# Kernel tuning notes

Hardware: AMD Instinct MI355X
Metric: run time of the kernel (lower is better)

The kernel has to match this reference:

```python
import jax, jax.numpy as jnp
import numpy as np

PI = 3.141592653589793
TAU = 2.0      # tau for both rpe_lif (spikingjelly default 2.0) and act_conv (params['tau'])
V_TH = 1.0     # spikingjelly LIFNode default v_threshold
EPS = 1e-5     # LayerNorm / BatchNorm eps


@jax.custom_vjp
def atan_spike(x):
    # Heaviside forward, ATan surrogate backward (spikingjelly surrogate.ATan, alpha=2)
    return (x >= 0.0).astype(x.dtype)

def _atan_fwd(x):
    return atan_spike(x), x

def _atan_bwd(x, g):
    # (alpha/2) / (1 + ((pi/2)*alpha*x)^2) with alpha=2 -> 1/(1+(pi*x)^2)
    return (g / (1.0 + (PI * x) ** 2),)

atan_spike.defvjp(_atan_fwd, _atan_bwd)


def lif(x_seq, tau=TAU):
    """Multi-step LIF: decay_input=True, v_reset=0, hard reset, detach_reset.
    x_seq: [T, ...]; returns spikes [T, ...]."""
    def step(v, x):
        v = v + (x - v) / tau                      # neuronal charge
        s = atan_spike(v - V_TH)                   # fire
        v = v * (1.0 - jax.lax.stop_gradient(s))   # detached hard reset to 0
        return v, s
    _, spikes = jax.lax.scan(step, jnp.zeros_like(x_seq[0]), x_seq)
    return spikes


def setup_inputs() -> dict:
    key = jax.random.key(0)
    ks = jax.random.split(key, 8)
    B, L, D, T = 256, 50, 128, 4
    n_items, n_h, n_v = 100001, 8, 4
    emb = jax.random.normal(ks[0], (n_items, D), jnp.float32) * 0.5
    emb = emb.at[0].set(0.0)  # padding_idx=0
    return {
        "item_seq": jax.random.randint(ks[1], (B, L), 0, n_items, jnp.int32),
        "emb_table": emb,
        "ln_gamma": jnp.ones((D,), jnp.float32),
        "ln_beta": jnp.zeros((D,), jnp.float32),
        "conv_v_w": jax.random.normal(ks[2], (n_v, L), jnp.float32) * float(1.0 / np.sqrt(L)),
        # per-length kernels stored padded: kernel for length k=i+1 is conv_h_w[i, :, :k, :]
        "conv_h_w": jax.random.normal(ks[3], (L, n_h, L, D), jnp.float32) * 0.02,
        "bn_gamma": jnp.ones((L, n_h), jnp.float32),
        "bn_beta": jnp.zeros((L, n_h), jnp.float32),
        "fc_h_w": jax.random.normal(ks[4], (D, n_h * L), jnp.float32) * 0.05,
        "fc_h_b": jnp.zeros((D,), jnp.float32),
        "fc_v_w": jax.random.normal(ks[5], (D, n_v * D), jnp.float32) * 0.04,
        "fc_v_b": jnp.zeros((D,), jnp.float32),
        "T": 4,
    }


def reference(item_seq, emb_table, ln_gamma, ln_beta, conv_v_w, conv_h_w,
              bn_gamma, bn_beta, fc_h_w, fc_h_b, fc_v_w, fc_v_b, T):
    B, L = item_seq.shape
    D = emb_table.shape[1]
    n_h = conv_h_w.shape[1]
    n_v = conv_v_w.shape[0]

    # embedding + LayerNorm
    emb = emb_table[item_seq]                                   # [B,L,D]
    mu = emb.mean(-1, keepdims=True)
    var = emb.var(-1, keepdims=True)
    x = (emb - mu) / jnp.sqrt(var + EPS) * ln_gamma + ln_beta   # [B,L,D]

    # repeat over T and spike (rpe_lif)
    s = lif(jnp.broadcast_to(x, (T, B, L, D)))                  # binary spikes [T,B,L,D]

    # vertical conv: kernel (L,1), no bias -> collapses seq axis
    out_v = jnp.einsum('tbld,cl->tbcd', s, conv_v_w).reshape(T, B, n_v * D)

    # horizontal multi-scale convs + BN(train stats) + LIF + global max pool
    s2 = s.reshape(T * B, 1, L, D)
    pools = []
    for i in range(L):
        k = i + 1
        w = conv_h_w[i, :, :k, :][:, None]                      # [n_h,1,k,D]
        y = jax.lax.conv_general_dilated(
            s2, w, (1, 1), 'VALID',
            dimension_numbers=('NCHW', 'OIHW', 'NCHW'))[:, :, :, 0]  # [TB,n_h,L-k+1]
        m = y.mean(axis=(0, 2))                                  # BN over (T*B, spatial)
        v = y.var(axis=(0, 2))
        y = (y - m[:, None]) * (bn_gamma[i][:, None] / jnp.sqrt(v[:, None] + EPS)) + bn_beta[i][:, None]
        y = lif(y.reshape(T, B, n_h, L - k + 1))                 # [T,B,n_h,L-k+1]
        pools.append(y.max(axis=-1))                             # [T,B,n_h]
    out_h = jnp.concatenate(pools, axis=-1)                      # [T,B,n_h*L]

    out_h = (out_h @ fc_h_w.T + fc_h_b).mean(0)                  # [B,D]
    out_v = out_v.mean(0) @ fc_v_w.T + fc_v_b                    # [B,D]
    return out_h + out_v
```

## Files before the change

### kernel.cpp

```cpp
#include <hip/hip_runtime.h>

#define B_ 256
#define L_ 50
#define D_ 128
#define T_ 4
#define NH 8
#define NV 4
#define TB_ (T_*B_)
#define EPSF 1e-5f

typedef _Float16 h8 __attribute__((ext_vector_type(8)));
typedef float f4 __attribute__((ext_vector_type(4)));

__device__ __forceinline__ float waveSum(float v) {
    #pragma unroll
    for (int o = 32; o > 0; o >>= 1) v += __shfl_down(v, o, 64);
    return v;
}

__device__ __forceinline__ size_t yoff(int i) {
    return (size_t)8192 * (size_t)(50 * i - (i * (i - 1)) / 2);
}

__global__ __launch_bounds__(256) void k0_wsplit(
        const float* __restrict__ w, _Float16* __restrict__ whl) {
    int dk = blockIdx.x, i = blockIdx.y;
    int t = threadIdx.x;
    int c = t >> 4, gd = t & 15;
    int h = c & 7;
    bool live = (i < 50) && (dk <= i);
    const float* src = w + (((size_t)i * NH + h) * L_ + dk) * D_ + gd * 8;
    h8 o;
    #pragma unroll
    for (int e = 0; e < 8; ++e) {
        float wv = live ? src[e] : 0.f;
        _Float16 hi = (_Float16)wv;
        o[e] = (c < 8) ? hi : (_Float16)((wv - (float)hi) * 1024.f);
    }
    *(h8*)(whl + (((size_t)i * 50 + dk) * 16 + c) * 128 + ((gd ^ c) & 15) * 8) = o;
}

__global__ __launch_bounds__(128) void k1_embed_ln_lif(
        const int* __restrict__ item, const float* __restrict__ tab,
        const float* __restrict__ g, const float* __restrict__ be,
        _Float16* __restrict__ s16, float* __restrict__ smean) {
    int bid = blockIdx.x;
    int b = bid / L_, l = bid % L_;
    int d = threadIdx.x;
    int wid = d >> 6, lane = d & 63;
    __shared__ float red[2];
    int it = item[b * L_ + l];
    float e = tab[(size_t)it * D_ + d];
    float sm_ = waveSum(e);
    if (lane == 0) red[wid] = sm_;
    __syncthreads();
    float mu = (red[0] + red[1]) * (1.f / 128.f);
    __syncthreads();
    float df = e - mu;
    float s2 = waveSum(df * df);
    if (lane == 0) red[wid] = s2;
    __syncthreads();
    float var = (red[0] + red[1]) * (1.f / 128.f);
    float x = df / sqrtf(var + EPSF) * g[d] + be[d];
    float v = 0.f, acc = 0.f;
    int pos = (((d >> 3) ^ l) & 15) * 8 + (d & 7);
    #pragma unroll
    for (int t = 0; t < T_; ++t) {
        v += (x - v) * 0.5f;
        float sp = (v >= 1.f) ? 1.f : 0.f;
        v *= (1.f - sp);
        s16[((size_t)(t * B_ + b) * L_ + l) * D_ + pos] = (_Float16)sp;
        acc += sp;
    }
    smean[((size_t)b * L_ + l) * D_ + d] = acc * 0.25f;
}

template<int MTG>
__global__ __launch_bounds__(512, 2) void k2v(
        const _Float16* __restrict__ s16, const _Float16* __restrict__ whl,
        float* __restrict__ y, int gbase, int joff) {
    extern __shared__ __align__(16) char lds[];
    char* B0 = lds + 102400;
    const int tbo = blockIdx.x;
    const int i0 = (gbase + blockIdx.y) * 4;
    const int kmax = (i0 + 4 <= 50) ? (i0 + 4) : 50;
    const int tid = threadIdx.x;
    const int wave = tid >> 6, lane = tid & 63;
    const int tq = wave >> 2;
    const int dc = wave & 3;
    const int c_ = lane & 15, g = lane >> 4;

    {
        const float4* src = (const float4*)(s16 + (size_t)tbo * 8 * (L_ * D_));
        float4* dst = (float4*)lds;
        for (int idx = tid; idx < 6400; idx += 512) dst[idx] = src[idx];
    }
    const char* bsrc = (const char*)whl + (size_t)i0 * 50 * 4096;
    const int o0 = tid * 16, o1 = 8192 + tid * 16;
    const char* g0p = bsrc + (size_t)(o0 >> 12) * (50 * 4096) + (o0 & 4095);
    const char* g1p = bsrc + (size_t)(o1 >> 12) * (50 * 4096) + (o1 & 4095);
    float4 n0 = *(const float4*)(g0p);
    float4 n1 = *(const float4*)(g1p);
    __syncthreads();
    *(float4*)(B0 + o0) = n0;
    *(float4*)(B0 + o1) = n1;
    __syncthreads();

    f4 acc[4][4][MTG];
    #pragma unroll
    for (int sc = 0; sc < 4; ++sc)
        #pragma unroll
        for (int tt = 0; tt < 4; ++tt)
            #pragma unroll
            for (int jt = 0; jt < MTG; ++jt) { f4 z = {0.f, 0.f, 0.f, 0.f}; acc[sc][tt][jt] = z; }

    const int boffc = c_ * 256 + ((((dc << 2) + g) ^ c_) & 15) * 16;
    for (int dk = 0; dk < kmax; ++dk) {
        const bool more = (dk + 1 < kmax);
        float4 m0, m1;
        if (more) {
            m0 = *(const float4*)(g0p + (size_t)(dk + 1) * 4096);
            m1 = *(const float4*)(g1p + (size_t)(dk + 1) * 4096);
        }
        __builtin_amdgcn_sched_barrier(0);
        const char* Bs = B0 + (dk & 1) * 16384;
        h8 bf[4];
        #pragma unroll
        for (int sc = 0; sc < 4; ++sc)
            bf[sc] = *(const h8*)(Bs + sc * 4096 + boffc);
        #pragma unroll
        for (int tt = 0; tt < 4; ++tt) {
            const int tbL = tq * 4 + tt;
            #pragma unroll
            for (int jt = 0; jt < MTG; ++jt) {
                int l = (joff + jt) * 16 + c_ + dk; if (l > 49) l = 49;
                h8 a = *(const h8*)(lds + tbL * 12800 + l * 256 +
                                    ((((dc << 2) + g) ^ l) & 15) * 16);
                #pragma unroll
                for (int sc = 0; sc < 4; ++sc)
                    acc[sc][tt][jt] = __builtin_amdgcn_mfma_f32_16x16x32_f16(a, bf[sc], acc[sc][tt][jt], 0, 0, 0);
            }
        }
        if (more) {
            char* Bn = B0 + ((dk + 1) & 1) * 16384;
            *(float4*)(Bn + o0) = m0;
            *(float4*)(Bn + o1) = m1;
        }
        __syncthreads();
    }

    f4* mbuf = (f4*)lds;
    #pragma unroll
    for (int jt = 0; jt < MTG; ++jt) {
        __syncthreads();
        if (dc != 0) {
            f4* wp = mbuf + (size_t)(((dc - 1) * 2 + tq) * 16) * 64 + lane;
            #pragma unroll
            for (int sc = 0; sc < 4; ++sc)
                #pragma unroll
                for (int tt = 0; tt < 4; ++tt)
                    wp[(sc * 4 + tt) * 64] = acc[sc][tt][jt];
        }
        __syncthreads();
        if (dc == 0) {
            #pragma unroll
            for (int dd = 0; dd < 3; ++dd) {
                const f4* rp = mbuf + (size_t)((dd * 2 + tq) * 16) * 64 + lane;
                #pragma unroll
                for (int sc = 0; sc < 4; ++sc)
                    #pragma unroll
                    for (int tt = 0; tt < 4; ++tt)
                        acc[sc][tt][jt] += rp[(sc * 4 + tt) * 64];
            }
        }
    }

    if (dc == 0) {
        const bool hiLane = (c_ < 8);
        const int h = c_ & 7;
        #pragma unroll
        for (int sc = 0; sc < 4; ++sc) {
            const int i = i0 + sc;
            const int J = 50 - i;
            if (J <= 0) continue;
            #pragma unroll
            for (int tt = 0; tt < 4; ++tt) {
                const int tb = tbo * 8 + tq * 4 + tt;
                size_t yb = yoff(i) + ((size_t)tb * NH + h) * J;
                #pragma unroll
                for (int jt = 0; jt < MTG; ++jt) {
                    #pragma unroll
                    for (int r = 0; r < 4; ++r) {
                        float lo = __shfl_xor(acc[sc][tt][jt][r], 8, 64);
                        int j = (joff + jt) * 16 + g * 4 + r;
                        if (hiLane && j < J) y[yb + j] = acc[sc][tt][jt][r] + lo * (1.f / 1024.f);
                    }
                }
            }
        }
    }
}

__global__ __launch_bounds__(256) void k3_partial(
        const float* __restrict__ y, float* __restrict__ psum) {
    int ih = blockIdx.x, ck = blockIdx.y;
    int i = ih >> 3, h = ih & 7;
    int J = 50 - i;
    size_t yb = yoff(i);
    int tid = threadIdx.x;
    int grp = tid >> 5, sub = tid & 31;
    float sm = 0.f, ss = 0.f;
    for (int tb = ck * 128 + grp; tb < (ck + 1) * 128; tb += 8) {
        const float* row = y + yb + ((size_t)tb * NH + h) * J;
        for (int j = sub; j < J; j += 32) { float v = row[j]; sm += v; ss += v * v; }
    }
    __shared__ float r1[4], r2[4];
    float a = waveSum(sm), b = waveSum(ss);
    int wid = tid >> 6, lane = tid & 63;
    if (lane == 0) { r1[wid] = a; r2[wid] = b; }
    __syncthreads();
    if (tid == 0) {
        psum[((size_t)ih * 8 + ck) * 2]     = r1[0] + r1[1] + r1[2] + r1[3];
        psum[((size_t)ih * 8 + ck) * 2 + 1] = r2[0] + r2[1] + r2[2] + r2[3];
    }
}

__global__ __launch_bounds__(256) void k3_final(
        const float* __restrict__ psum, const float* __restrict__ bng,
        float* __restrict__ statm, float* __restrict__ stats_) {
    int ih = blockIdx.x * 256 + threadIdx.x;
    if (ih >= 400) return;
    float S = 0.f, Q = 0.f;
    for (int ck = 0; ck < 8; ++ck) {
        S += psum[((size_t)ih * 8 + ck) * 2];
        Q += psum[((size_t)ih * 8 + ck) * 2 + 1];
    }
    int i = ih >> 3;
    float cnt = 1024.f * (float)(50 - i);
    float m = S / cnt;
    float var = Q / cnt - m * m; if (var < 0.f) var = 0.f;
    statm[ih] = m;
    stats_[ih] = bng[ih] / sqrtf(var + EPSF);
}

__global__ __launch_bounds__(512) void k4_bn_lif_pool(
        const float* __restrict__ y, const float* __restrict__ statm,
        const float* __restrict__ stats_, const float* __restrict__ bnb,
        float* __restrict__ ps) {
    int b = blockIdx.x, i = blockIdx.y, J = L_ - i;
    int h = threadIdx.x >> 6, lane = threadIdx.x & 63;
    int ih = i * NH + h;
    float m = statm[ih], sc = stats_[ih], bb = bnb[ih];
    size_t yb = yoff(i);
    bool valid = lane < J;
    float v = 0.f; int cnt = 0;
    #pragma unroll
    for (int t = 0; t < T_; ++t) {
        int tb = t * B_ + b;
        float yn;
        if (valid) {
            float raw = y[yb + ((size_t)tb * NH + h) * J + lane];
            yn = (raw - m) * sc + bb;
        } else yn = -1e30f;
        v += (yn - v) * 0.5f;
        bool sp = (v >= 1.f);
        if (sp) v = 0.f;
        if (__any(sp)) cnt++;
    }
    if (lane == 0) ps[(size_t)b * 400 + ih] = (float)cnt;
}

__global__ __launch_bounds__(128) void k5_final(
        const float* __restrict__ smean, const float* __restrict__ ps,
        const float* __restrict__ convv, const float* __restrict__ fchw,
        const float* __restrict__ fchb, const float* __restrict__ fcvw,
        const float* __restrict__ fcvb, float* __restrict__ out) {
    __shared__ float sm_l[L_ * D_];
    __shared__ float vm[NV * D_];
    __shared__ float ps_l[400];
    int b = blockIdx.x, tid = threadIdx.x;
    for (int idx = tid; idx < L_ * D_; idx += 128) sm_l[idx] = smean[(size_t)b * (L_ * D_) + idx];
    for (int idx = tid; idx < 400; idx += 128) ps_l[idx] = ps[(size_t)b * 400 + idx];
    __syncthreads();
    int d = tid;
    #pragma unroll
    for (int c = 0; c < NV; ++c) {
        float a = 0.f;
        for (int l = 0; l < L_; ++l) a += convv[c * L_ + l] * sm_l[l * D_ + d];
        vm[c * D_ + d] = a;
    }
    __syncthreads();
    float acc = fchb[d] + fcvb[d];
    float ah = 0.f;
    for (int ih = 0; ih < 400; ++ih) ah += ps_l[ih] * fchw[d * 400 + ih];
    acc += ah * 0.25f;
    float av = 0.f;
    for (int cd = 0; cd < NV * D_; ++cd) av += vm[cd] * fcvw[d * (NV * D_) + cd];
    acc += av;
    out[(size_t)b * D_ + d] = acc;
}

extern "C" void kernel_launch(void* const* d_in, const int* in_sizes, int n_in,
                              void* d_out, int out_size, void* d_ws, size_t ws_size,
                              hipStream_t stream) {
    const int*   item  = (const int*)d_in[0];
    const float* tab   = (const float*)d_in[1];
    const float* lng   = (const float*)d_in[2];
    const float* lnb   = (const float*)d_in[3];
    const float* convv = (const float*)d_in[4];
    const float* convh = (const float*)d_in[5];
    const float* bng   = (const float*)d_in[6];
    const float* bnb   = (const float*)d_in[7];
    const float* fchw  = (const float*)d_in[8];
    const float* fchb  = (const float*)d_in[9];
    const float* fcvw  = (const float*)d_in[10];
    const float* fcvb  = (const float*)d_in[11];
    float* out = (float*)d_out;

    char* ws = (char*)d_ws;
    _Float16* s16  = (_Float16*)(ws);
    float* smean   = (float*)(ws + 13107200LL);
    float* y       = (float*)(ws + 19660800LL);
    _Float16* whl  = (_Float16*)(ws + 61440000LL);
    float* statm   = (float*)(ws + 72089600LL);
    float* stats_  = (float*)(ws + 72091200LL);
    float* ps      = (float*)(ws + 72092800LL);
    float* psum    = (float*)(ws + 72502400LL);

    hipFuncSetAttribute(reinterpret_cast<const void*>(&k2v<1>),
        hipFuncAttributeMaxDynamicSharedMemorySize, 135168);
    hipFuncSetAttribute(reinterpret_cast<const void*>(&k2v<2>),
        hipFuncAttributeMaxDynamicSharedMemorySize, 135168);
    hipFuncSetAttribute(reinterpret_cast<const void*>(&k2v<3>),
        hipFuncAttributeMaxDynamicSharedMemorySize, 135168);

    k0_wsplit<<<dim3(50, 52), 256, 0, stream>>>(convh, whl);
    k1_embed_ln_lif<<<B_ * L_, 128, 0, stream>>>(item, tab, lng, lnb, s16, smean);
    k2v<2><<<dim3(128, 1), 512, 135168, stream>>>(s16, whl, y, 0, 0);
    k2v<2><<<dim3(128, 1), 512, 135168, stream>>>(s16, whl, y, 0, 2);
    k2v<3><<<dim3(128, 4), 512, 135168, stream>>>(s16, whl, y, 1, 0);
    k2v<2><<<dim3(128, 4), 512, 135168, stream>>>(s16, whl, y, 5, 0);
    k2v<1><<<dim3(128, 4), 512, 135168, stream>>>(s16, whl, y, 9, 0);
    k3_partial<<<dim3(400, 8), 256, 0, stream>>>(y, psum);
    k3_final<<<dim3(2, 1), 256, 0, stream>>>(psum, bng, statm, stats_);
    k4_bn_lif_pool<<<dim3(B_, L_), 512, 0, stream>>>(y, statm, stats_, bnb, ps);
    k5_final<<<B_, 128, 0, stream>>>(smean, ps, convv, fchw, fchb, fcvw, fcvb, out);
}
```

Baseline: 320.5 us.

## Load conv weight fragments directly from global into registers, dropping LDS staging

The horizontal-conv MFMA kernel no longer stages the B (weight) tile through a double-buffered LDS region with per-step barriers. Each lane now loads its four h8 weight fragments straight from global memory, prefetching the next step into registers. This removes the per-iteration __syncthreads and LDS writes, and cuts dynamic LDS to 102400 bytes. The MTG=3 launch is split into MTG=2 and MTG=1 launches, likely to limit register pressure. The cost is redundant global/L2 reads of the weights across waves and one more kernel launch.

```diff
diff --git a/kernel.cpp b/kernel.cpp
--- a/kernel.cpp
+++ b/kernel.cpp
@@ -76,11 +76,10 @@
 }
 
 template<int MTG>
-__global__ __launch_bounds__(512, 2) void k2v(
+__global__ __launch_bounds__(512, 2) void k2w(
         const _Float16* __restrict__ s16, const _Float16* __restrict__ whl,
         float* __restrict__ y, int gbase, int joff) {
     extern __shared__ __align__(16) char lds[];
-    char* B0 = lds + 102400;
     const int tbo = blockIdx.x;
     const int i0 = (gbase + blockIdx.y) * 4;
     const int kmax = (i0 + 4 <= 50) ? (i0 + 4) : 50;
@@ -95,15 +94,14 @@
         float4* dst = (float4*)lds;
         for (int idx = tid; idx < 6400; idx += 512) dst[idx] = src[idx];
     }
-    const char* bsrc = (const char*)whl + (size_t)i0 * 50 * 4096;
-    const int o0 = tid * 16, o1 = 8192 + tid * 16;
-    const char* g0p = bsrc + (size_t)(o0 >> 12) * (50 * 4096) + (o0 & 4095);
-    const char* g1p = bsrc + (size_t)(o1 >> 12) * (50 * 4096) + (o1 & 4095);
-    float4 n0 = *(const float4*)(g0p);
-    float4 n1 = *(const float4*)(g1p);
-    __syncthreads();
-    *(float4*)(B0 + o0) = n0;
-    *(float4*)(B0 + o1) = n1;
+
+    const int boffc = c_ * 256 + ((((dc << 2) + g) ^ c_) & 15) * 16;
+    const char* gB = (const char*)whl + (size_t)i0 * 204800 + boffc;
+
+    h8 bf0 = *(const h8*)(gB);
+    h8 bf1 = *(const h8*)(gB + 204800);
+    h8 bf2 = *(const h8*)(gB + 409600);
+    h8 bf3 = *(const h8*)(gB + 614400);
     __syncthreads();
 
     f4 acc[4][4][MTG];
@@ -114,20 +112,16 @@
             #pragma unroll
             for (int jt = 0; jt < MTG; ++jt) { f4 z = {0.f, 0.f, 0.f, 0.f}; acc[sc][tt][jt] = z; }
 
-    const int boffc = c_ * 256 + ((((dc << 2) + g) ^ c_) & 15) * 16;
     for (int dk = 0; dk < kmax; ++dk) {
         const bool more = (dk + 1 < kmax);
-        float4 m0, m1;
+        h8 bn0, bn1, bn2, bn3;
         if (more) {
-            m0 = *(const float4*)(g0p + (size_t)(dk + 1) * 4096);
-            m1 = *(const float4*)(g1p + (size_t)(dk + 1) * 4096);
-        }
-        __builtin_amdgcn_sched_barrier(0);
-        const char* Bs = B0 + (dk & 1) * 16384;
-        h8 bf[4];
-        #pragma unroll
-        for (int sc = 0; sc < 4; ++sc)
-            bf[sc] = *(const h8*)(Bs + sc * 4096 + boffc);
+            const char* p = gB + (size_t)(dk + 1) * 4096;
+            bn0 = *(const h8*)(p);
+            bn1 = *(const h8*)(p + 204800);
+            bn2 = *(const h8*)(p + 409600);
+            bn3 = *(const h8*)(p + 614400);
+        }
         #pragma unroll
         for (int tt = 0; tt < 4; ++tt) {
             const int tbL = tq * 4 + tt;
@@ -136,17 +130,13 @@
                 int l = (joff + jt) * 16 + c_ + dk; if (l > 49) l = 49;
                 h8 a = *(const h8*)(lds + tbL * 12800 + l * 256 +
                                     ((((dc << 2) + g) ^ l) & 15) * 16);
-                #pragma unroll
-                for (int sc = 0; sc < 4; ++sc)
-                    acc[sc][tt][jt] = __builtin_amdgcn_mfma_f32_16x16x32_f16(a, bf[sc], acc[sc][tt][jt], 0, 0, 0);
+                acc[0][tt][jt] = __builtin_amdgcn_mfma_f32_16x16x32_f16(a, bf0, acc[0][tt][jt], 0, 0, 0);
+                acc[1][tt][jt] = __builtin_amdgcn_mfma_f32_16x16x32_f16(a, bf1, acc[1][tt][jt], 0, 0, 0);
+                acc[2][tt][jt] = __builtin_amdgcn_mfma_f32_16x16x32_f16(a, bf2, acc[2][tt][jt], 0, 0, 0);
+                acc[3][tt][jt] = __builtin_amdgcn_mfma_f32_16x16x32_f16(a, bf3, acc[3][tt][jt], 0, 0, 0);
             }
         }
-        if (more) {
-            char* Bn = B0 + ((dk + 1) & 1) * 16384;
-            *(float4*)(Bn + o0) = m0;
-            *(float4*)(Bn + o1) = m1;
-        }
-        __syncthreads();
+        bf0 = bn0; bf1 = bn1; bf2 = bn2; bf3 = bn3;
     }
 
     f4* mbuf = (f4*)lds;
@@ -327,20 +317,19 @@
     float* ps      = (float*)(ws + 72092800LL);
     float* psum    = (float*)(ws + 72502400LL);
 
-    hipFuncSetAttribute(reinterpret_cast<const void*>(&k2v<1>),
-        hipFuncAttributeMaxDynamicSharedMemorySize, 135168);
-    hipFuncSetAttribute(reinterpret_cast<const void*>(&k2v<2>),
-        hipFuncAttributeMaxDynamicSharedMemorySize, 135168);
-    hipFuncSetAttribute(reinterpret_cast<const void*>(&k2v<3>),
-        hipFuncAttributeMaxDynamicSharedMemorySize, 135168);
+    hipFuncSetAttribute(reinterpret_cast<const void*>(&k2w<1>),
+        hipFuncAttributeMaxDynamicSharedMemorySize, 102400);
+    hipFuncSetAttribute(reinterpret_cast<const void*>(&k2w<2>),
+        hipFuncAttributeMaxDynamicSharedMemorySize, 102400);
 
     k0_wsplit<<<dim3(50, 52), 256, 0, stream>>>(convh, whl);
     k1_embed_ln_lif<<<B_ * L_, 128, 0, stream>>>(item, tab, lng, lnb, s16, smean);
-    k2v<2><<<dim3(128, 1), 512, 135168, stream>>>(s16, whl, y, 0, 0);
-    k2v<2><<<dim3(128, 1), 512, 135168, stream>>>(s16, whl, y, 0, 2);
-    k2v<3><<<dim3(128, 4), 512, 135168, stream>>>(s16, whl, y, 1, 0);
-    k2v<2><<<dim3(128, 4), 512, 135168, stream>>>(s16, whl, y, 5, 0);
-    k2v<1><<<dim3(128, 4), 512, 135168, stream>>>(s16, whl, y, 9, 0);
+    k2w<2><<<dim3(128, 1), 512, 102400, stream>>>(s16, whl, y, 0, 0);
+    k2w<2><<<dim3(128, 1), 512, 102400, stream>>>(s16, whl, y, 0, 2);
+    k2w<2><<<dim3(128, 4), 512, 102400, stream>>>(s16, whl, y, 1, 0);
+    k2w<1><<<dim3(128, 4), 512, 102400, stream>>>(s16, whl, y, 1, 2);
+    k2w<2><<<dim3(128, 4), 512, 102400, stream>>>(s16, whl, y, 5, 0);
+    k2w<1><<<dim3(128, 4), 512, 102400, stream>>>(s16, whl, y, 9, 0);
     k3_partial<<<dim3(400, 8), 256, 0, stream>>>(y, psum);
     k3_final<<<dim3(2, 1), 256, 0, stream>>>(psum, bng, statm, stats_);
     k4_bn_lif_pool<<<dim3(B_, L_), 512, 0, stream>>>(y, statm, stats_, bnb, ps);
```

Measured after the change: 320.4 us. Within noise of the previous version (-0.0%).
